# Kernel tuning notes

Measured on AMD Instinct MI355X. Metric: run time of the kernel, lower is better.

The kernel has to match this reference:

```python
import jax, jax.numpy as jnp
import numpy as np

B, S, D = 2, 4096, 768
H, HD = 12, 64  # num_head, head_dim


def setup_inputs() -> dict:
    key = jax.random.key(0)
    ks = jax.random.split(key, 10)
    s = 0.02
    return {
        "X": jax.random.normal(ks[0], (B, S, D), dtype=jnp.float32),
        "mask": jnp.ones((B, S), dtype=jnp.float32),
        "Wq": jax.random.normal(ks[1], (D, H * HD), dtype=jnp.float32) * s,
        "bq": jnp.zeros((H * HD,), dtype=jnp.float32),
        "Wk": jax.random.normal(ks[2], (D, H * HD), dtype=jnp.float32) * s,
        "bk": jnp.zeros((H * HD,), dtype=jnp.float32),
        "Wv": jax.random.normal(ks[3], (D, H * HD), dtype=jnp.float32) * s,
        "bv": jnp.zeros((H * HD,), dtype=jnp.float32),
        "Wo": jax.random.normal(ks[4], (H * HD, D), dtype=jnp.float32) * s,
        "bo": jnp.zeros((D,), dtype=jnp.float32),
    }


def _split_heads(x):
    # [B,S,H*HD] -> [B,H,S,HD]
    return x.reshape(B, S, H, HD).transpose(0, 2, 1, 3)


def reference(X, mask, Wq, bq, Wk, bk, Wv, bv, Wo, bo):
    Q = _split_heads(X @ Wq + bq)
    K = _split_heads(X @ Wk + bk)
    V = _split_heads(X @ Wv + bv)
    # scores: [B,H,S,S]
    dot = jnp.einsum("bhqd,bhkd->bhqk", Q, K) / np.sqrt(HD).astype(np.float32)
    dot = dot - 1e6 * (1.0 - mask[:, None, None, :])
    attn = jax.nn.softmax(dot, axis=-1)
    ctx = jnp.einsum("bhqk,bhkd->bhqd", attn, V)
    # combine heads: [B,H,S,HD] -> [B,S,H*HD]
    ctx = ctx.transpose(0, 2, 1, 3).reshape(B, S, H * HD)
    return ctx @ Wo + bo
```

## Files before the change

### kernel.cpp

```cpp
#include <hip/hip_runtime.h>

#define BATCH   2
#define S_LEN   4096
#define D_MODEL 768
#define NH      12
#define HDIM    64
#define MROWS   (BATCH * S_LEN)
#define QBLK    128
#define KVBLK   64
#define NT      (S_LEN / KVBLK)
#define LOG2E   1.4426950408889634f

typedef float f32x4  __attribute__((ext_vector_type(4)));
typedef float f32x16 __attribute__((ext_vector_type(16)));
typedef short bf16x8 __attribute__((ext_vector_type(8)));

#if __has_builtin(__builtin_amdgcn_exp2f)
#define EXP2(x) __builtin_amdgcn_exp2f(x)
#else
#define EXP2(x) exp2f(x)
#endif

static __device__ __forceinline__ unsigned short f2bf(float f) {
  union { float f; unsigned u; } v; v.f = f;
  unsigned r = v.u + 0x7fffu + ((v.u >> 16) & 1u);
  return (unsigned short)(r >> 16);
}

static __device__ __forceinline__ unsigned cvtpk(float lo, float hi) {
  unsigned r;
  asm("v_cvt_pk_bf16_f32 %0, %1, %2" : "=v"(r) : "v"(lo), "v"(hi));
  return r;
}

template <int BASE>
static __device__ __forceinline__ bf16x8 pack_frag(const f32x16& s) {
  unsigned a0 = cvtpk(s[BASE + 0], s[BASE + 1]);
  unsigned b0 = cvtpk(s[BASE + 4], s[BASE + 5]);
  asm("v_permlane32_swap_b32 %0, %1" : "+v"(a0), "+v"(b0));
  unsigned a1 = cvtpk(s[BASE + 2], s[BASE + 3]);
  unsigned b1 = cvtpk(s[BASE + 6], s[BASE + 7]);
  asm("v_permlane32_swap_b32 %0, %1" : "+v"(a1), "+v"(b1));
  union { unsigned w[4]; bf16x8 v; } u;
  u.w[0] = a0; u.w[1] = a1; u.w[2] = b0; u.w[3] = b1;
  return u.v;
}

#define Z16 {0.f,0.f,0.f,0.f,0.f,0.f,0.f,0.f,0.f,0.f,0.f,0.f,0.f,0.f,0.f,0.f}


__global__ void conv_x(const float* __restrict__ X, unsigned short* __restrict__ Xb) {
  int i = blockIdx.x * blockDim.x + threadIdx.x;
  float4 v = ((const float4*)X)[i];
  ushort4 o;
  o.x = f2bf(v.x); o.y = f2bf(v.y); o.z = f2bf(v.z); o.w = f2bf(v.w);
  ((ushort4*)Xb)[i] = o;
}

__global__ __launch_bounds__(1024) void mask_prep(const float* __restrict__ mask,
                                                  float* __restrict__ madd,
                                                  int* __restrict__ flag) {
  __shared__ int ok[16];
  int t = threadIdx.x;
  int all1 = 1;
  #pragma unroll
  for (int i = 0; i < MROWS / 1024; ++i) {
    int idx = i * 1024 + t;
    float m = mask[idx];
    madd[idx] = (-1e6f * LOG2E) * (1.0f - m);
    all1 &= (m == 1.0f);
  }
  all1 = __all(all1) ? 1 : 0;
  if ((t & 63) == 0) ok[t >> 6] = all1;
  __syncthreads();
  if (t == 0) {
    int a = 1;
    #pragma unroll
    for (int i = 0; i < 16; ++i) a &= ok[i];
    *flag = a;
  }
}

__global__ __launch_bounds__(256) void trans_w(
    const float* __restrict__ W0, const float* __restrict__ W1,
    const float* __restrict__ W2, const float* __restrict__ W3,
    unsigned short* __restrict__ T0, unsigned short* __restrict__ T1,
    unsigned short* __restrict__ T2, unsigned short* __restrict__ T3) {
  const float* W; unsigned short* T;
  int zz = blockIdx.z;
  if (zz == 0) { W = W0; T = T0; }
  else if (zz == 1) { W = W1; T = T1; }
  else if (zz == 2) { W = W2; T = T2; }
  else { W = W3; T = T3; }
  __shared__ float tile[32][33];
  int tx = threadIdx.x & 31, ty = threadIdx.x >> 5;
  int bx = blockIdx.x * 32, by = blockIdx.y * 32;
  #pragma unroll
  for (int i = ty; i < 32; i += 8) tile[i][tx] = W[(size_t)(by + i) * D_MODEL + bx + tx];
  __syncthreads();
  #pragma unroll
  for (int i = ty; i < 32; i += 8)
    T[(size_t)(bx + i) * D_MODEL + by + tx] = f2bf(tile[tx][i]);
}

__global__ __launch_bounds__(256) void qkv_gemm(
    const unsigned short* __restrict__ Xb,
    const unsigned short* __restrict__ Wqt, const unsigned short* __restrict__ Wkt,
    const unsigned short* __restrict__ Wvt,
    const float* __restrict__ bq, const float* __restrict__ bk, const float* __restrict__ bv,
    unsigned short* __restrict__ Qo, unsigned short* __restrict__ Ko,
    unsigned short* __restrict__ Vto) {
  __shared__ unsigned short As[64][72];
  __shared__ unsigned short Bs[64][72];
  int zz = blockIdx.z;
  const unsigned short* Wt = zz == 0 ? Wqt : (zz == 1 ? Wkt : Wvt);
  const float* bias = zz == 0 ? bq : (zz == 1 ? bk : bv);
  int tid = threadIdx.x;
  int w = tid >> 6, l = tid & 63, lr = l & 15, lg = l >> 4;
  int mb = blockIdx.x * 64, nb = blockIdx.y * 64;
  int srow = tid >> 2, scol = (tid & 3) * 16;
  f32x4 acc[4];
  #pragma unroll
  for (int i = 0; i < 4; ++i) acc[i] = (f32x4){0.f, 0.f, 0.f, 0.f};
  for (int kb = 0; kb < D_MODEL / 64; ++kb) {
    __syncthreads();
    *(uint4*)&As[srow][scol]     = *(const uint4*)(Xb + (size_t)(mb + srow) * D_MODEL + kb * 64 + scol);
    *(uint4*)&As[srow][scol + 8] = *(const uint4*)(Xb + (size_t)(mb + srow) * D_MODEL + kb * 64 + scol + 8);
    *(uint4*)&Bs[srow][scol]     = *(const uint4*)(Wt + (size_t)(nb + srow) * D_MODEL + kb * 64 + scol);
    *(uint4*)&Bs[srow][scol + 8] = *(const uint4*)(Wt + (size_t)(nb + srow) * D_MODEL + kb * 64 + scol + 8);
    __syncthreads();
    #pragma unroll
    for (int kk = 0; kk < 2; ++kk) {
      bf16x8 af = *(const bf16x8*)(&As[w * 16 + lr][kk * 32 + lg * 8]);
      #pragma unroll
      for (int ct = 0; ct < 4; ++ct) {
        bf16x8 bfv = *(const bf16x8*)(&Bs[ct * 16 + lr][kk * 32 + lg * 8]);
        acc[ct] = __builtin_amdgcn_mfma_f32_16x16x32_bf16(af, bfv, acc[ct], 0, 0, 0);
      }
    }
  }
  #pragma unroll
  for (int ct = 0; ct < 4; ++ct) {
    int n = nb + ct * 16 + lr;
    float bia = bias[n];
    int h = n >> 6, hd = n & 63;
    #pragma unroll
    for (int r = 0; r < 4; ++r) {
      int m = mb + w * 16 + lg * 4 + r;
      int b = m >> 12, s = m & 4095;
      float val = acc[ct][r] + bia;
      if (zz == 0)
        Qo[((size_t)(b * NH + h) * S_LEN + s) * HDIM + hd] = f2bf(val * 0.125f * LOG2E);
      else if (zz == 1)
        Ko[((size_t)(b * NH + h) * S_LEN + s) * HDIM + hd] = f2bf(val);
      else
        Vto[((size_t)(b * NH + h) * HDIM + hd) * S_LEN + s] = f2bf(val);
    }
  }
}

__global__ __launch_bounds__(256) void attn_kernel(
    const unsigned short* __restrict__ Q, const unsigned short* __restrict__ K,
    const unsigned short* __restrict__ Vt, const float* __restrict__ madd,
    const int* __restrict__ allones_p, unsigned short* __restrict__ Ctx) {
  __shared__ unsigned short Ks[2][64][72];
  __shared__ unsigned short Vs[2][64][72];
  int lin = blockIdx.x;
  int wg = (lin & 7) * 96 + (lin >> 3);
  int qb = wg & 31, bh = wg >> 5;
  int b = bh / NH, h = bh % NH;
  int tid = threadIdx.x;
  int w = tid >> 6, lane = tid & 63;
  int lq = lane & 31, hi = lane >> 5;
  const unsigned short* Qb = Q + (size_t)bh * S_LEN * HDIM;
  const unsigned short* Kb = K + (size_t)bh * S_LEN * HDIM;
  const unsigned short* Vb = Vt + (size_t)bh * HDIM * S_LEN;
  const float* maddb = madd + (size_t)b * S_LEN;
  const int allones = *allones_p;

  int qrow = qb * QBLK + w * 32 + lq;
  bf16x8 qf0 = *(const bf16x8*)(Qb + (size_t)qrow * HDIM + 0 * 16 + hi * 8);
  bf16x8 qf1 = *(const bf16x8*)(Qb + (size_t)qrow * HDIM + 1 * 16 + hi * 8);
  bf16x8 qf2 = *(const bf16x8*)(Qb + (size_t)qrow * HDIM + 2 * 16 + hi * 8);
  bf16x8 qf3 = *(const bf16x8*)(Qb + (size_t)qrow * HDIM + 3 * 16 + hi * 8);

  f32x16 acc0 = Z16, acc1 = Z16;
  float m_run = -3.0e38f, l_run = 0.f;

  int srow = tid >> 3, sseg = (tid & 7) * 8;
  uint4 ka, kc, va, vc;

  ka = *(const uint4*)(Kb + (size_t)srow * HDIM + sseg);
  kc = *(const uint4*)(Kb + (size_t)(srow + 32) * HDIM + sseg);
  va = *(const uint4*)(Vb + (size_t)srow * S_LEN + sseg);
  vc = *(const uint4*)(Vb + (size_t)(srow + 32) * S_LEN + sseg);
  *(uint4*)&Ks[0][srow][sseg]      = ka;
  *(uint4*)&Ks[0][srow + 32][sseg] = kc;
  *(uint4*)&Vs[0][srow][sseg]      = va;
  *(uint4*)&Vs[0][srow + 32][sseg] = vc;
  __syncthreads();

  for (int t = 0; t < NT; ++t) {
    int cur = t & 1;
    int kbase = t * KVBLK;
    if (t + 1 < NT) {
      int nb2 = kbase + KVBLK;
      ka = *(const uint4*)(Kb + (size_t)(nb2 + srow) * HDIM + sseg);
      kc = *(const uint4*)(Kb + (size_t)(nb2 + srow + 32) * HDIM + sseg);
      va = *(const uint4*)(Vb + (size_t)srow * S_LEN + nb2 + sseg);
      vc = *(const uint4*)(Vb + (size_t)(srow + 32) * S_LEN + nb2 + sseg);
    }
    f32x16 s0 = Z16, s1 = Z16;
    #pragma unroll
    for (int c = 0; c < 4; ++c) {
      bf16x8 kf0 = *(const bf16x8*)(&Ks[cur][lq][c * 16 + hi * 8]);
      bf16x8 kf1 = *(const bf16x8*)(&Ks[cur][32 + lq][c * 16 + hi * 8]);
      bf16x8 qf = c == 0 ? qf0 : (c == 1 ? qf1 : (c == 2 ? qf2 : qf3));
      s0 = __builtin_amdgcn_mfma_f32_32x32x16_bf16(kf0, qf, s0, 0, 0, 0);
      s1 = __builtin_amdgcn_mfma_f32_32x32x16_bf16(kf1, qf, s1, 0, 0, 0);
    }
    if (!allones) {
      #pragma unroll
      for (int g = 0; g < 4; ++g) {
        float4 m0 = *(const float4*)(maddb + kbase + g * 8 + hi * 4);
        float4 m1 = *(const float4*)(maddb + kbase + 32 + g * 8 + hi * 4);
        s0[g * 4 + 0] += m0.x; s0[g * 4 + 1] += m0.y;
        s0[g * 4 + 2] += m0.z; s0[g * 4 + 3] += m0.w;
        s1[g * 4 + 0] += m1.x; s1[g * 4 + 1] += m1.y;
        s1[g * 4 + 2] += m1.z; s1[g * 4 + 3] += m1.w;
      }
    }
    float tt[8];
    #pragma unroll
    for (int i = 0; i < 8; ++i)
      tt[i] = fmaxf(fmaxf(s0[i], s0[i + 8]), fmaxf(s1[i], s1[i + 8]));
    float pm = fmaxf(fmaxf(fmaxf(tt[0], tt[1]), fmaxf(tt[2], tt[3])),
                     fmaxf(fmaxf(tt[4], tt[5]), fmaxf(tt[6], tt[7])));
    pm = fmaxf(pm, __shfl_xor(pm, 32, 64));
    if (__any(pm > m_run + 8.f)) {
      float mnew = fmaxf(m_run, pm);
      float alpha = EXP2(m_run - mnew);
      m_run = mnew;
      l_run *= alpha;
      #pragma unroll
      for (int r = 0; r < 16; ++r) {
        float ar = __shfl(alpha, (r & 3) + 8 * (r >> 2) + 4 * hi, 64);
        acc0[r] *= ar; acc1[r] *= ar;
      }
    }
    float psA = 0.f, psB = 0.f, psC = 0.f, psD = 0.f;
    #pragma unroll
    for (int r = 0; r < 4; ++r) {
      s0[r]      = EXP2(s0[r] - m_run);      psA += s0[r];
      s0[r + 4]  = EXP2(s0[r + 4] - m_run);  psB += s0[r + 4];
      s0[r + 8]  = EXP2(s0[r + 8] - m_run);  psC += s0[r + 8];
      s0[r + 12] = EXP2(s0[r + 12] - m_run); psD += s0[r + 12];
    }
    #pragma unroll
    for (int r = 0; r < 4; ++r) {
      s1[r]      = EXP2(s1[r] - m_run);      psA += s1[r];
      s1[r + 4]  = EXP2(s1[r + 4] - m_run);  psB += s1[r + 4];
      s1[r + 8]  = EXP2(s1[r + 8] - m_run);  psC += s1[r + 8];
      s1[r + 12] = EXP2(s1[r + 12] - m_run); psD += s1[r + 12];
    }
    float psum = (psA + psB) + (psC + psD);
    psum += __shfl_xor(psum, 32, 64);
    l_run += psum;
    bf16x8 pa0 = pack_frag<0>(s0);
    bf16x8 pa1 = pack_frag<8>(s0);
    bf16x8 pa2 = pack_frag<0>(s1);
    bf16x8 pa3 = pack_frag<8>(s1);
    #pragma unroll
    for (int c = 0; c < 4; ++c) {
      bf16x8 pa = c == 0 ? pa0 : (c == 1 ? pa1 : (c == 2 ? pa2 : pa3));
      bf16x8 vf0 = *(const bf16x8*)(&Vs[cur][lq][c * 16 + hi * 8]);
      bf16x8 vf1 = *(const bf16x8*)(&Vs[cur][32 + lq][c * 16 + hi * 8]);
      acc0 = __builtin_amdgcn_mfma_f32_32x32x16_bf16(pa, vf0, acc0, 0, 0, 0);
      acc1 = __builtin_amdgcn_mfma_f32_32x32x16_bf16(pa, vf1, acc1, 0, 0, 0);
    }
    if (t + 1 < NT) {
      int nxt = cur ^ 1;
      *(uint4*)&Ks[nxt][srow][sseg]      = ka;
      *(uint4*)&Ks[nxt][srow + 32][sseg] = kc;
      *(uint4*)&Vs[nxt][srow][sseg]      = va;
      *(uint4*)&Vs[nxt][srow + 32][sseg] = vc;
      __syncthreads();
    }
  }
  #pragma unroll
  for (int r = 0; r < 16; ++r) {
    int qr = (r & 3) + 8 * (r >> 2) + 4 * hi;
    float lv = __shfl(l_run, qr, 64);
    float rl = 1.0f / lv;
    int qglob = qb * QBLK + w * 32 + qr;
    size_t base = ((size_t)(b * S_LEN + qglob)) * D_MODEL + h * HDIM;
    Ctx[base + lq]      = f2bf(acc0[r] * rl);
    Ctx[base + 32 + lq] = f2bf(acc1[r] * rl);
  }
}

__global__ __launch_bounds__(256) void out_gemm(
    const unsigned short* __restrict__ Ctx, const unsigned short* __restrict__ Wot,
    const float* __restrict__ bo, float* __restrict__ Out) {
  __shared__ unsigned short As[64][72];
  __shared__ unsigned short Bs[64][72];
  int tid = threadIdx.x;
  int w = tid >> 6, l = tid & 63, lr = l & 15, lg = l >> 4;
  int mb = blockIdx.x * 64, nb = blockIdx.y * 64;
  int srow = tid >> 2, scol = (tid & 3) * 16;
  f32x4 acc[4];
  #pragma unroll
  for (int i = 0; i < 4; ++i) acc[i] = (f32x4){0.f, 0.f, 0.f, 0.f};
  for (int kb = 0; kb < D_MODEL / 64; ++kb) {
    __syncthreads();
    *(uint4*)&As[srow][scol]     = *(const uint4*)(Ctx + (size_t)(mb + srow) * D_MODEL + kb * 64 + scol);
    *(uint4*)&As[srow][scol + 8] = *(const uint4*)(Ctx + (size_t)(mb + srow) * D_MODEL + kb * 64 + scol + 8);
    *(uint4*)&Bs[srow][scol]     = *(const uint4*)(Wot + (size_t)(nb + srow) * D_MODEL + kb * 64 + scol);
    *(uint4*)&Bs[srow][scol + 8] = *(const uint4*)(Wot + (size_t)(nb + srow) * D_MODEL + kb * 64 + scol + 8);
    __syncthreads();
    #pragma unroll
    for (int kk = 0; kk < 2; ++kk) {
      bf16x8 af = *(const bf16x8*)(&As[w * 16 + lr][kk * 32 + lg * 8]);
      #pragma unroll
      for (int ct = 0; ct < 4; ++ct) {
        bf16x8 bfv = *(const bf16x8*)(&Bs[ct * 16 + lr][kk * 32 + lg * 8]);
        acc[ct] = __builtin_amdgcn_mfma_f32_16x16x32_bf16(af, bfv, acc[ct], 0, 0, 0);
      }
    }
  }
  #pragma unroll
  for (int ct = 0; ct < 4; ++ct) {
    int n = nb + ct * 16 + lr;
    float bia = bo[n];
    #pragma unroll
    for (int r = 0; r < 4; ++r) {
      int m = mb + w * 16 + lg * 4 + r;
      Out[(size_t)m * D_MODEL + n] = acc[ct][r] + bia;
    }
  }
}


extern "C" void kernel_launch(void* const* d_in, const int* in_sizes, int n_in,
                              void* d_out, int out_size, void* d_ws, size_t ws_size,
                              hipStream_t stream) {
  const float* X    = (const float*)d_in[0];
  const float* mask = (const float*)d_in[1];
  const float* Wq   = (const float*)d_in[2];
  const float* bq   = (const float*)d_in[3];
  const float* Wk   = (const float*)d_in[4];
  const float* bk   = (const float*)d_in[5];
  const float* Wv   = (const float*)d_in[6];
  const float* bv   = (const float*)d_in[7];
  const float* Wo   = (const float*)d_in[8];
  const float* bo   = (const float*)d_in[9];
  float* out = (float*)d_out;
  char* ws = (char*)d_ws;

  const size_t XB_OFF   = 0;
  const size_t WQT_OFF  = 12582912;
  const size_t WKT_OFF  = WQT_OFF + 1179648;
  const size_t WVT_OFF  = WKT_OFF + 1179648;
  const size_t WOT_OFF  = WVT_OFF + 1179648;
  const size_t Q_OFF    = WOT_OFF + 1179648;
  const size_t K_OFF    = Q_OFF + 12582912;
  const size_t VT_OFF   = K_OFF + 12582912;
  const size_t CTX_OFF  = VT_OFF + 12582912;
  const size_t MADD_OFF = CTX_OFF + 12582912;
  const size_t FLAG_OFF = MADD_OFF + MROWS * 4;

  unsigned short* Xb  = (unsigned short*)(ws + XB_OFF);
  unsigned short* Wqt = (unsigned short*)(ws + WQT_OFF);
  unsigned short* Wkt = (unsigned short*)(ws + WKT_OFF);
  unsigned short* Wvt = (unsigned short*)(ws + WVT_OFF);
  unsigned short* Wot = (unsigned short*)(ws + WOT_OFF);
  unsigned short* Qw  = (unsigned short*)(ws + Q_OFF);
  unsigned short* Kw  = (unsigned short*)(ws + K_OFF);
  unsigned short* Vtw = (unsigned short*)(ws + VT_OFF);
  unsigned short* Ctx = (unsigned short*)(ws + CTX_OFF);
  float* madd = (float*)(ws + MADD_OFF);
  int* flag   = (int*)(ws + FLAG_OFF);

  conv_x<<<dim3(MROWS * D_MODEL / 4 / 256), 256, 0, stream>>>(X, Xb);
  mask_prep<<<dim3(1), 1024, 0, stream>>>(mask, madd, flag);
  trans_w<<<dim3(24, 24, 4), 256, 0, stream>>>(Wq, Wk, Wv, Wo, Wqt, Wkt, Wvt, Wot);
  qkv_gemm<<<dim3(MROWS / 64, D_MODEL / 64, 3), 256, 0, stream>>>(
      Xb, Wqt, Wkt, Wvt, bq, bk, bv, Qw, Kw, Vtw);
  attn_kernel<<<dim3((S_LEN / QBLK) * (BATCH * NH)), 256, 0, stream>>>(
      Qw, Kw, Vtw, madd, flag, Ctx);
  out_gemm<<<dim3(MROWS / 64, D_MODEL / 64), 256, 0, stream>>>(Ctx, Wot, bo, out);
}
```

Baseline: 271.4 us.

## Use 128x128 GEMM tiles with direct global-to-LDS loads and MFMA priority hints

Both projection GEMMs move from 64x64 to 128x128 block tiles, with each wave computing a 4x4 grid of 16x16 MFMA tiles. Shared-memory staging now uses global_load_lds, so data goes straight from global memory to LDS without passing through registers. This raises operand reuse per LDS load and cuts the number of blocks and load instructions. The attention kernel also wraps its MFMA sections in s_setprio so the matrix instructions get issue priority. The unpadded LDS layout can cause bank conflicts, and the larger accumulator array raises register pressure.

```diff
diff --git a/kernel.cpp b/kernel.cpp
--- a/kernel.cpp
+++ b/kernel.cpp
@@ -31,6 +31,13 @@
   unsigned r;
   asm("v_cvt_pk_bf16_f32 %0, %1, %2" : "=v"(r) : "v"(lo), "v"(hi));
   return r;
+}
+
+typedef __attribute__((address_space(1))) const unsigned int as1_cuint;
+typedef __attribute__((address_space(3))) unsigned int as3_uint;
+static __device__ __forceinline__ void gload_lds16(const unsigned short* g,
+                                                   unsigned short* l) {
+  __builtin_amdgcn_global_load_lds((as1_cuint*)g, (as3_uint*)l, 16, 0, 0);
 }
 
 template <int BASE>
@@ -110,51 +117,67 @@
     const float* __restrict__ bq, const float* __restrict__ bk, const float* __restrict__ bv,
     unsigned short* __restrict__ Qo, unsigned short* __restrict__ Ko,
     unsigned short* __restrict__ Vto) {
-  __shared__ unsigned short As[64][72];
-  __shared__ unsigned short Bs[64][72];
+  __shared__ unsigned short As[128 * 64];
+  __shared__ unsigned short Bs[128 * 64];
   int zz = blockIdx.z;
   const unsigned short* Wt = zz == 0 ? Wqt : (zz == 1 ? Wkt : Wvt);
   const float* bias = zz == 0 ? bq : (zz == 1 ? bk : bv);
   int tid = threadIdx.x;
-  int w = tid >> 6, l = tid & 63, lr = l & 15, lg = l >> 4;
-  int mb = blockIdx.x * 64, nb = blockIdx.y * 64;
-  int srow = tid >> 2, scol = (tid & 3) * 16;
-  f32x4 acc[4];
-  #pragma unroll
-  for (int i = 0; i < 4; ++i) acc[i] = (f32x4){0.f, 0.f, 0.f, 0.f};
+  int w = tid >> 6, lane = tid & 63, lr = lane & 15, lg = lane >> 4;
+  int wr = w >> 1, wc = w & 1;
+  int mb = blockIdx.x * 128, nb = blockIdx.y * 128;
+  const unsigned short* Ag = Xb + (size_t)(mb + (tid >> 3)) * D_MODEL + (tid & 7) * 8;
+  const unsigned short* Bg = Wt + (size_t)(nb + (tid >> 3)) * D_MODEL + (tid & 7) * 8;
+  unsigned short* Al = As + (size_t)tid * 8;
+  unsigned short* Bl = Bs + (size_t)tid * 8;
+  f32x4 acc[4][4];
+  #pragma unroll
+  for (int m = 0; m < 4; ++m)
+    #pragma unroll
+    for (int n = 0; n < 4; ++n) acc[m][n] = (f32x4){0.f, 0.f, 0.f, 0.f};
   for (int kb = 0; kb < D_MODEL / 64; ++kb) {
     __syncthreads();
-    *(uint4*)&As[srow][scol]     = *(const uint4*)(Xb + (size_t)(mb + srow) * D_MODEL + kb * 64 + scol);
-    *(uint4*)&As[srow][scol + 8] = *(const uint4*)(Xb + (size_t)(mb + srow) * D_MODEL + kb * 64 + scol + 8);
-    *(uint4*)&Bs[srow][scol]     = *(const uint4*)(Wt + (size_t)(nb + srow) * D_MODEL + kb * 64 + scol);
-    *(uint4*)&Bs[srow][scol + 8] = *(const uint4*)(Wt + (size_t)(nb + srow) * D_MODEL + kb * 64 + scol + 8);
+    #pragma unroll
+    for (int i = 0; i < 4; ++i) {
+      gload_lds16(Ag + (size_t)(i * 32) * D_MODEL + kb * 64, Al + i * 2048);
+      gload_lds16(Bg + (size_t)(i * 32) * D_MODEL + kb * 64, Bl + i * 2048);
+    }
     __syncthreads();
     #pragma unroll
     for (int kk = 0; kk < 2; ++kk) {
-      bf16x8 af = *(const bf16x8*)(&As[w * 16 + lr][kk * 32 + lg * 8]);
-      #pragma unroll
-      for (int ct = 0; ct < 4; ++ct) {
-        bf16x8 bfv = *(const bf16x8*)(&Bs[ct * 16 + lr][kk * 32 + lg * 8]);
-        acc[ct] = __builtin_amdgcn_mfma_f32_16x16x32_bf16(af, bfv, acc[ct], 0, 0, 0);
+      bf16x8 af[4], bfv[4];
+      #pragma unroll
+      for (int m = 0; m < 4; ++m)
+        af[m] = *(const bf16x8*)(As + (wr * 64 + m * 16 + lr) * 64 + kk * 32 + lg * 8);
+      #pragma unroll
+      for (int n = 0; n < 4; ++n)
+        bfv[n] = *(const bf16x8*)(Bs + (wc * 64 + n * 16 + lr) * 64 + kk * 32 + lg * 8);
+      #pragma unroll
+      for (int m = 0; m < 4; ++m)
+        #pragma unroll
+        for (int n = 0; n < 4; ++n)
+          acc[m][n] = __builtin_amdgcn_mfma_f32_16x16x32_bf16(af[m], bfv[n], acc[m][n], 0, 0, 0);
+    }
+  }
+  #pragma unroll
+  for (int n = 0; n < 4; ++n) {
+    int nc = nb + wc * 64 + n * 16 + lr;
+    float bia = bias[nc];
+    int h = nc >> 6, hd = nc & 63;
+    #pragma unroll
+    for (int m = 0; m < 4; ++m) {
+      #pragma unroll
+      for (int r = 0; r < 4; ++r) {
+        int mr = mb + wr * 64 + m * 16 + lg * 4 + r;
+        int b = mr >> 12, s = mr & 4095;
+        float val = acc[m][n][r] + bia;
+        if (zz == 0)
+          Qo[((size_t)(b * NH + h) * S_LEN + s) * HDIM + hd] = f2bf(val * 0.125f * LOG2E);
+        else if (zz == 1)
+          Ko[((size_t)(b * NH + h) * S_LEN + s) * HDIM + hd] = f2bf(val);
+        else
+          Vto[((size_t)(b * NH + h) * HDIM + hd) * S_LEN + s] = f2bf(val);
       }
-    }
-  }
-  #pragma unroll
-  for (int ct = 0; ct < 4; ++ct) {
-    int n = nb + ct * 16 + lr;
-    float bia = bias[n];
-    int h = n >> 6, hd = n & 63;
-    #pragma unroll
-    for (int r = 0; r < 4; ++r) {
-      int m = mb + w * 16 + lg * 4 + r;
-      int b = m >> 12, s = m & 4095;
-      float val = acc[ct][r] + bia;
-      if (zz == 0)
-        Qo[((size_t)(b * NH + h) * S_LEN + s) * HDIM + hd] = f2bf(val * 0.125f * LOG2E);
-      else if (zz == 1)
-        Ko[((size_t)(b * NH + h) * S_LEN + s) * HDIM + hd] = f2bf(val);
-      else
-        Vto[((size_t)(b * NH + h) * HDIM + hd) * S_LEN + s] = f2bf(val);
     }
   }
 }
@@ -211,6 +234,7 @@
       vc = *(const uint4*)(Vb + (size_t)(srow + 32) * S_LEN + nb2 + sseg);
     }
     f32x16 s0 = Z16, s1 = Z16;
+    __builtin_amdgcn_s_setprio(1);
     #pragma unroll
     for (int c = 0; c < 4; ++c) {
       bf16x8 kf0 = *(const bf16x8*)(&Ks[cur][lq][c * 16 + hi * 8]);
@@ -219,6 +243,7 @@
       s0 = __builtin_amdgcn_mfma_f32_32x32x16_bf16(kf0, qf, s0, 0, 0, 0);
       s1 = __builtin_amdgcn_mfma_f32_32x32x16_bf16(kf1, qf, s1, 0, 0, 0);
     }
+    __builtin_amdgcn_s_setprio(0);
     if (!allones) {
       #pragma unroll
       for (int g = 0; g < 4; ++g) {
@@ -270,6 +295,7 @@
     bf16x8 pa1 = pack_frag<8>(s0);
     bf16x8 pa2 = pack_frag<0>(s1);
     bf16x8 pa3 = pack_frag<8>(s1);
+    __builtin_amdgcn_s_setprio(1);
     #pragma unroll
     for (int c = 0; c < 4; ++c) {
       bf16x8 pa = c == 0 ? pa0 : (c == 1 ? pa1 : (c == 2 ? pa2 : pa3));
@@ -278,6 +304,7 @@
       acc0 = __builtin_amdgcn_mfma_f32_32x32x16_bf16(pa, vf0, acc0, 0, 0, 0);
       acc1 = __builtin_amdgcn_mfma_f32_32x32x16_bf16(pa, vf1, acc1, 0, 0, 0);
     }
+    __builtin_amdgcn_s_setprio(0);
     if (t + 1 < NT) {
       int nxt = cur ^ 1;
       *(uint4*)&Ks[nxt][srow][sseg]      = ka;
@@ -302,40 +329,56 @@
 __global__ __launch_bounds__(256) void out_gemm(
     const unsigned short* __restrict__ Ctx, const unsigned short* __restrict__ Wot,
     const float* __restrict__ bo, float* __restrict__ Out) {
-  __shared__ unsigned short As[64][72];
-  __shared__ unsigned short Bs[64][72];
+  __shared__ unsigned short As[128 * 64];
+  __shared__ unsigned short Bs[128 * 64];
   int tid = threadIdx.x;
-  int w = tid >> 6, l = tid & 63, lr = l & 15, lg = l >> 4;
-  int mb = blockIdx.x * 64, nb = blockIdx.y * 64;
-  int srow = tid >> 2, scol = (tid & 3) * 16;
-  f32x4 acc[4];
-  #pragma unroll
-  for (int i = 0; i < 4; ++i) acc[i] = (f32x4){0.f, 0.f, 0.f, 0.f};
+  int w = tid >> 6, lane = tid & 63, lr = lane & 15, lg = lane >> 4;
+  int wr = w >> 1, wc = w & 1;
+  int mb = blockIdx.x * 128, nb = blockIdx.y * 128;
+  const unsigned short* Ag = Ctx + (size_t)(mb + (tid >> 3)) * D_MODEL + (tid & 7) * 8;
+  const unsigned short* Bg = Wot + (size_t)(nb + (tid >> 3)) * D_MODEL + (tid & 7) * 8;
+  unsigned short* Al = As + (size_t)tid * 8;
+  unsigned short* Bl = Bs + (size_t)tid * 8;
+  f32x4 acc[4][4];
+  #pragma unroll
+  for (int m = 0; m < 4; ++m)
+    #pragma unroll
+    for (int n = 0; n < 4; ++n) acc[m][n] = (f32x4){0.f, 0.f, 0.f, 0.f};
   for (int kb = 0; kb < D_MODEL / 64; ++kb) {
     __syncthreads();
-    *(uint4*)&As[srow][scol]     = *(const uint4*)(Ctx + (size_t)(mb + srow) * D_MODEL + kb * 64 + scol);
-    *(uint4*)&As[srow][scol + 8] = *(const uint4*)(Ctx + (size_t)(mb + srow) * D_MODEL + kb * 64 + scol + 8);
-    *(uint4*)&Bs[srow][scol]     = *(const uint4*)(Wot + (size_t)(nb + srow) * D_MODEL + kb * 64 + scol);
-    *(uint4*)&Bs[srow][scol + 8] = *(const uint4*)(Wot + (size_t)(nb + srow) * D_MODEL + kb * 64 + scol + 8);
+    #pragma unroll
+    for (int i = 0; i < 4; ++i) {
+      gload_lds16(Ag + (size_t)(i * 32) * D_MODEL + kb * 64, Al + i * 2048);
+      gload_lds16(Bg + (size_t)(i * 32) * D_MODEL + kb * 64, Bl + i * 2048);
+    }
     __syncthreads();
     #pragma unroll
     for (int kk = 0; kk < 2; ++kk) {
-      bf16x8 af = *(const bf16x8*)(&As[w * 16 + lr][kk * 32 + lg * 8]);
-      #pragma unroll
-      for (int ct = 0; ct < 4; ++ct) {
-        bf16x8 bfv = *(const bf16x8*)(&Bs[ct * 16 + lr][kk * 32 + lg * 8]);
-        acc[ct] = __builtin_amdgcn_mfma_f32_16x16x32_bf16(af, bfv, acc[ct], 0, 0, 0);
+      bf16x8 af[4], bfv[4];
+      #pragma unroll
+      for (int m = 0; m < 4; ++m)
+        af[m] = *(const bf16x8*)(As + (wr * 64 + m * 16 + lr) * 64 + kk * 32 + lg * 8);
+      #pragma unroll
+      for (int n = 0; n < 4; ++n)
+        bfv[n] = *(const bf16x8*)(Bs + (wc * 64 + n * 16 + lr) * 64 + kk * 32 + lg * 8);
+      #pragma unroll
+      for (int m = 0; m < 4; ++m)
+        #pragma unroll
+        for (int n = 0; n < 4; ++n)
+          acc[m][n] = __builtin_amdgcn_mfma_f32_16x16x32_bf16(af[m], bfv[n], acc[m][n], 0, 0, 0);
+    }
+  }
+  #pragma unroll
+  for (int n = 0; n < 4; ++n) {
+    int nc = nb + wc * 64 + n * 16 + lr;
+    float bia = bo[nc];
+    #pragma unroll
+    for (int m = 0; m < 4; ++m) {
+      #pragma unroll
+      for (int r = 0; r < 4; ++r) {
+        int mr = mb + wr * 64 + m * 16 + lg * 4 + r;
+        Out[(size_t)mr * D_MODEL + nc] = acc[m][n][r] + bia;
       }
-    }
-  }
-  #pragma unroll
-  for (int ct = 0; ct < 4; ++ct) {
-    int n = nb + ct * 16 + lr;
-    float bia = bo[n];
-    #pragma unroll
-    for (int r = 0; r < 4; ++r) {
-      int m = mb + w * 16 + lg * 4 + r;
-      Out[(size_t)m * D_MODEL + n] = acc[ct][r] + bia;
     }
   }
 }
@@ -384,9 +427,9 @@
   conv_x<<<dim3(MROWS * D_MODEL / 4 / 256), 256, 0, stream>>>(X, Xb);
   mask_prep<<<dim3(1), 1024, 0, stream>>>(mask, madd, flag);
   trans_w<<<dim3(24, 24, 4), 256, 0, stream>>>(Wq, Wk, Wv, Wo, Wqt, Wkt, Wvt, Wot);
-  qkv_gemm<<<dim3(MROWS / 64, D_MODEL / 64, 3), 256, 0, stream>>>(
+  qkv_gemm<<<dim3(MROWS / 128, D_MODEL / 128, 3), 256, 0, stream>>>(
       Xb, Wqt, Wkt, Wvt, bq, bk, bv, Qw, Kw, Vtw);
   attn_kernel<<<dim3((S_LEN / QBLK) * (BATCH * NH)), 256, 0, stream>>>(
       Qw, Kw, Vtw, madd, flag, Ctx);
-  out_gemm<<<dim3(MROWS / 64, D_MODEL / 64), 256, 0, stream>>>(Ctx, Wot, bo, out);
-}
+  out_gemm<<<dim3(MROWS / 128, D_MODEL / 128), 256, 0, stream>>>(Ctx, Wot, bo, out);
+}
```

Result: slower. 282.6 us (+4.1%).
